# Optimization experiments

Hardware: AMD Instinct MI355X
Metric: run time of the kernel (lower is better)

## Reference

```python
import jax, jax.numpy as jnp
import numpy as np

N, E, H, ED = 50000, 400000, 512, 64
BN_EPS = 1e-5


def setup_inputs() -> dict:
    key = jax.random.key(0)
    ks = jax.random.split(key, 8)
    s = lambda d: 1.0 / np.sqrt(d)
    return {
        "x": jax.random.normal(ks[0], (N, H), jnp.float32),
        "edge_attr": jax.random.normal(ks[1], (E, ED), jnp.float32),
        "edge_index": jax.random.randint(ks[2], (2, E), 0, N, jnp.int32),
        # GINEConv edge projection (edge_dim -> hidden_dim)
        "W_e": jax.random.normal(ks[3], (ED, H), jnp.float32) * s(ED),
        "b_e": jnp.zeros((H,), jnp.float32),
        # 2-layer MLP: Linear(H, 2H) -> BN -> SiLU -> Linear(2H, H)
        "W1": jax.random.normal(ks[4], (H, 2 * H), jnp.float32) * s(H),
        "b1": jnp.zeros((2 * H,), jnp.float32),
        "g1": jnp.ones((2 * H,), jnp.float32),
        "beta1": jnp.zeros((2 * H,), jnp.float32),
        "W2": jax.random.normal(ks[5], (2 * H, H), jnp.float32) * s(2 * H),
        "b2": jnp.zeros((H,), jnp.float32),
        # outer BatchNorm(hidden_dim)
        "g2": jnp.ones((H,), jnp.float32),
        "beta2": jnp.zeros((H,), jnp.float32),
        # trainable GIN epsilon (init 0)
        "eps": jnp.zeros((), jnp.float32),
    }


def _bn(h, g, b):
    # training-mode batch norm over the node dimension (biased variance)
    mu = jnp.mean(h, axis=0)
    var = jnp.mean(jnp.square(h - mu), axis=0)
    return (h - mu) * jax.lax.rsqrt(var + BN_EPS) * g + b


def reference(x, edge_attr, edge_index, W_e, b_e, W1, b1, g1, beta1, W2, b2, g2, beta2, eps):
    src, dst = edge_index[0], edge_index[1]
    # message: ReLU(x_j + lin(e_ij)), gathered per edge  -> [E, H]
    msg = jax.nn.relu(x[src] + edge_attr @ W_e + b_e)
    # scatter-add aggregate into destination nodes -> [N, H]
    aggr = jax.ops.segment_sum(msg, dst, num_segments=x.shape[0])
    # GIN combine + 2-layer MLP with internal BatchNorm + SiLU (dropout=0)
    h = (1.0 + eps) * x + aggr
    h = jax.nn.silu(_bn(h @ W1 + b1, g1, beta1))
    h = h @ W2 + b2
    # outer BatchNorm + SiLU (dropout=0 -> identity)
    return jax.nn.silu(_bn(h, g2, beta2))
```

## Files before the change

kernel.cpp:

```cpp
#include <hip/hip_runtime.h>
#include <math.h>

#define NN 50000
#define NE 400000
#define HD 512
#define EDIM 64
#define H2 1024
#define LDT 72
#define CAP_SLOT 1200000
#define CAP_TILE 75000
#define CAP_HEAVY 8192
#define NBLK_SCAN 98

typedef short s16x8 __attribute__((ext_vector_type(8)));
typedef float f32x4 __attribute__((ext_vector_type(4)));

__device__ __forceinline__ unsigned short f2bf(float f) {
    union { float f; unsigned u; } v; v.f = f;
    unsigned r = v.u + 0x7fffu + ((v.u >> 16) & 1u);
    return (unsigned short)(r >> 16);
}
__device__ __forceinline__ float bf2f(unsigned short h) {
    union { unsigned u; float f; } v; v.u = ((unsigned)h) << 16;
    return v.f;
}
__device__ __forceinline__ float silu_f(float t) {
    return t / (1.f + __expf(-t));
}
__device__ __forceinline__ void gload_lds16(const unsigned short* g, unsigned short* l) {
    __builtin_amdgcn_global_load_lds(
        (const __attribute__((address_space(1))) unsigned int*)(g),
        (__attribute__((address_space(3))) unsigned int*)(l), 16, 0, 0);
}

constexpr size_t OFF_AGGRC = 0;
constexpr size_t OFF_XB   = 16777216;
constexpr size_t OFF_H1   = 0;
constexpr size_t OFF_H    = 102400000;
constexpr size_t OFF_WET  = 153600000;
constexpr size_t OFF_W1T  = OFF_WET + 65536;
constexpr size_t OFF_W2T  = OFF_W1T + 1048576;
constexpr size_t OFF_CNT  = OFF_W2T + 1048576;
constexpr size_t OFF_B1S  = OFF_CNT + 200000;
constexpr size_t OFF_B1Q  = OFF_B1S + 4096;
constexpr size_t OFF_B2S  = OFF_B1Q + 4096;
constexpr size_t OFF_B2Q  = OFF_B2S + 2048;
constexpr size_t ZERO_BYTES = 200000 + 4096 + 4096 + 2048 + 2048;
constexpr size_t OFF_TEX  = OFF_B2Q + 2048;
constexpr size_t OFF_BSUM = OFF_TEX + 200000;
constexpr size_t OFF_BOFF = OFF_BSUM + 512;
constexpr size_t OFF_T    = OFF_BOFF + 512;
constexpr size_t OFF_CUR  = OFF_T + 64;
constexpr size_t OFF_NOT  = OFF_CUR + 200000;
constexpr size_t OFF_SRCP = OFF_NOT + 300032;
constexpr size_t OFF_EIXP = OFF_SRCP + 4800000;
constexpr size_t OFF_SC1  = OFF_EIXP + 4800000;
constexpr size_t OFF_SB1  = OFF_SC1 + 4096;
constexpr size_t OFF_SC2  = OFF_SB1 + 4096;
constexpr size_t OFF_SB2  = OFF_SC2 + 2048;

__global__ __launch_bounds__(256) void k_convert(const float* __restrict__ We,
    const float* __restrict__ W1, const float* __restrict__ W2,
    unsigned short* __restrict__ wet, unsigned short* __restrict__ w1t,
    unsigned short* __restrict__ w2t) {
    int i = blockIdx.x * 256 + threadIdx.x;
    if (i < 32768) {
        int n = i >> 6, k = i & 63;
        wet[i] = f2bf(We[k * HD + n]);
    } else if (i < 32768 + 524288) {
        int j = i - 32768;
        int n = j >> 9, k = j & 511;
        w1t[j] = f2bf(W1[k * H2 + n]);
    } else if (i < 32768 + 2 * 524288) {
        int j = i - (32768 + 524288);
        int n = j >> 10, k = j & 1023;
        w2t[j] = f2bf(W2[k * HD + n]);
    }
}

__global__ __launch_bounds__(256) void k_xconv(const float* __restrict__ x,
    unsigned short* __restrict__ xb) {
    int t = blockIdx.x * 256 + threadIdx.x;
    if (t >= NN * 64) return;
    int n = t >> 6, rem = t & 63;
    int cb = rem >> 4, l = rem & 15;
    const float* src = x + (size_t)n * HD + cb * 128 + l;
    unsigned short o[8];
    #pragma unroll
    for (int j = 0; j < 8; ++j) o[j] = f2bf(src[j * 16]);
    *(uint4*)(xb + (size_t)n * HD + cb * 128 + l * 8) = *(const uint4*)o;
}

__global__ __launch_bounds__(256) void k_hist(const int* __restrict__ dst, int* __restrict__ counts) {
    int e = blockIdx.x * 256 + threadIdx.x;
    if (e < NE) atomicAdd(&counts[dst[e]], 1);
}

__global__ __launch_bounds__(512) void k_scan1(const int* __restrict__ counts,
    int* __restrict__ tile_excl, int* __restrict__ bsum) {
    __shared__ int wsums[8];
    int b = blockIdx.x, t = threadIdx.x;
    int i = b * 512 + t;
    int v = (i < NN) ? ((counts[i] + 15) >> 4) : 0;
    int lane = t & 63, wid = t >> 6;
    int x = v;
    #pragma unroll
    for (int o = 1; o < 64; o <<= 1) {
        int y = __shfl_up(x, o, 64);
        if (lane >= o) x += y;
    }
    if (lane == 63) wsums[wid] = x;
    __syncthreads();
    if (t == 0) {
        int run = 0;
        for (int w = 0; w < 8; ++w) { int tmp = wsums[w]; wsums[w] = run; run += tmp; }
    }
    __syncthreads();
    int excl = x - v + wsums[wid];
    if (i < NN) tile_excl[i] = excl;
    if (t == 511) bsum[b] = excl + v;
}

__global__ void k_scan2(const int* __restrict__ bsum, int* __restrict__ boff, int* __restrict__ Tout) {
    if (threadIdx.x == 0) {
        int run = 0;
        for (int b = 0; b < NBLK_SCAN; ++b) { boff[b] = run; run += bsum[b]; }
        Tout[0] = run;
        Tout[1] = 0;
    }
}

__global__ __launch_bounds__(512) void k_scan3(const int* __restrict__ counts,
    int* __restrict__ tile_excl, const int* __restrict__ boff,
    int* __restrict__ cursor, int* __restrict__ node_of_tile, int* __restrict__ Tout) {
    int b = blockIdx.x, t = threadIdx.x;
    int i = b * 512 + t;
    if (i >= NN) return;
    int tc = (counts[i] + 15) >> 4;
    int ts = tile_excl[i] + boff[b];
    cursor[i] = ts * 16;
    int hid = -1;
    if (tc > 1) {
        hid = atomicAdd(&Tout[1], 1);
        if (hid >= CAP_HEAVY) hid = CAP_HEAVY - 1;
    }
    tile_excl[i] = hid;
    unsigned tag = (tc > 1) ? (0x80000000u | (unsigned)hid) : (unsigned)i;
    for (int k = 0; k < tc; ++k) node_of_tile[ts + k] = (int)tag;
}

__global__ __launch_bounds__(256) void k_scatter(const int* __restrict__ src, const int* __restrict__ dst,
    int* __restrict__ cursor, int* __restrict__ srcp, int* __restrict__ eidxp) {
    int e = blockIdx.x * 256 + threadIdx.x;
    if (e < NE) {
        int d = dst[e];
        int p = atomicAdd(&cursor[d], 1);
        srcp[p] = src[e];
        eidxp[p] = e;
    }
}

__global__ __launch_bounds__(256, 4) void k_edge(
    const float* __restrict__ ea, const unsigned short* __restrict__ wet,
    const unsigned short* __restrict__ xb, const float* __restrict__ b_e,
    const float* __restrict__ eps,
    const int* __restrict__ srcp, const int* __restrict__ eidxp,
    const int* __restrict__ node_of_tile, const int* __restrict__ Tptr,
    float* __restrict__ aggrc, unsigned short* __restrict__ h) {
    int tile0 = blockIdx.x * 2;
    int T = Tptr[0];
    if (tile0 >= T) return;
    __shared__ unsigned short As[32 * LDT];
    __shared__ int Ss[32];
    __shared__ float Rs[4][128];
    int t = threadIdx.x;
    int slot0 = tile0 * 16;
    {
        int r = t >> 3, qq = t & 7;
        int s = srcp[slot0 + r];
        if (qq == 0) Ss[r] = s;
        unsigned short* lp = As + r * LDT + qq * 8;
        if (s >= 0) {
            int eix = eidxp[slot0 + r];
            const float* gp = ea + (size_t)eix * EDIM + qq * 8;
            float4 v0 = ((const float4*)gp)[0];
            float4 v1 = ((const float4*)gp)[1];
            lp[0] = f2bf(v0.x); lp[1] = f2bf(v0.y); lp[2] = f2bf(v0.z); lp[3] = f2bf(v0.w);
            lp[4] = f2bf(v1.x); lp[5] = f2bf(v1.y); lp[6] = f2bf(v1.z); lp[7] = f2bf(v1.w);
        } else {
            uint4 z = {0u, 0u, 0u, 0u};
            *(uint4*)lp = z;
        }
    }
    __syncthreads();
    int wave = t >> 6, lane = t & 63, l15 = lane & 15, quad = lane >> 4;
    int cblk = wave * 128;
    f32x4 acc[2][8];
    #pragma unroll
    for (int i = 0; i < 2; ++i)
        #pragma unroll
        for (int j = 0; j < 8; ++j) acc[i][j] = (f32x4){0.f, 0.f, 0.f, 0.f};
    #pragma unroll
    for (int k0 = 0; k0 < 64; k0 += 32) {
        s16x8 af[2], bfr[8];
        #pragma unroll
        for (int i = 0; i < 2; ++i)
            af[i] = *(const s16x8*)(As + (i * 16 + l15) * LDT + k0 + quad * 8);
        #pragma unroll
        for (int j = 0; j < 8; ++j)
            bfr[j] = *(const s16x8*)(wet + (size_t)(cblk + j * 16 + l15) * EDIM + k0 + quad * 8);
        #pragma unroll
        for (int i = 0; i < 2; ++i)
            #pragma unroll
            for (int j = 0; j < 8; ++j)
                acc[i][j] = __builtin_amdgcn_mfma_f32_16x16x32_bf16(af[i], bfr[j], acc[i][j], 0, 0, 0);
    }
    float ep = 1.0f + eps[0];
    float bev[8];
    #pragma unroll
    for (int j = 0; j < 8; ++j) bev[j] = b_e[cblk + j * 16 + l15];
    float* rp = Rs[wave];
    #pragma unroll
    for (int i = 0; i < 2; ++i) {
        int tile = tile0 + i;
        unsigned meta = (unsigned)node_of_tile[tile];
        int v = (int)(meta & 0x7fffffffu);
        int vc = v < NN ? v : 0;
        int srow = i * 16 + quad * 4;
        s16x8 xr[4]; float msk[4];
        #pragma unroll
        for (int r = 0; r < 4; ++r) {
            int s = Ss[srow + r];
            msk[r] = s >= 0 ? 1.f : 0.f;
            xr[r] = *(const s16x8*)(xb + (size_t)(s >= 0 ? s : 0) * HD + cblk + l15 * 8);
        }
        s16x8 xo = *(const s16x8*)(xb + (size_t)vc * HD + cblk + l15 * 8);
        float sum8[8];
        #pragma unroll
        for (int j = 0; j < 8; ++j) sum8[j] = 0.f;
        #pragma unroll
        for (int r = 0; r < 4; ++r) {
            #pragma unroll
            for (int j = 0; j < 8; ++j) {
                float vv = acc[i][j][r] + bf2f((unsigned short)xr[r][j]) + bev[j];
                vv = vv > 0.f ? vv : 0.f;
                sum8[j] = fmaf(msk[r], vv, sum8[j]);
            }
        }
        #pragma unroll
        for (int j = 0; j < 8; ++j) {
            sum8[j] += __shfl_xor(sum8[j], 16, 64);
            sum8[j] += __shfl_xor(sum8[j], 32, 64);
        }
        if (tile < T) {
            if (meta & 0x80000000u) {
                if (quad == 0) {
                    float* ap = aggrc + (size_t)v * HD + cblk;
                    #pragma unroll
                    for (int j = 0; j < 8; ++j) atomicAdd(ap + j * 16 + l15, sum8[j]);
                }
            } else {
                int j0 = quad * 2, j1 = j0 + 1;
                rp[j0 * 16 + l15] = fmaf(ep, bf2f((unsigned short)xo[j0]), sum8[j0]);
                rp[j1 * 16 + l15] = fmaf(ep, bf2f((unsigned short)xo[j1]), sum8[j1]);
                unsigned pk = (unsigned)f2bf(rp[lane * 2]) |
                              ((unsigned)f2bf(rp[lane * 2 + 1]) << 16);
                *(unsigned*)(h + (size_t)v * HD + cblk + lane * 2) = pk;
            }
        }
    }
}

__global__ __launch_bounds__(256) void k_combine_heavy(const float* __restrict__ aggrc,
    const float* __restrict__ x, const int* __restrict__ counts, const int* __restrict__ hidmap,
    const float* __restrict__ eps, unsigned short* __restrict__ h) {
    long i = ((long)blockIdx.x * 256 + threadIdx.x) * 4;
    if (i >= (long)NN * HD) return;
    int v = (int)(i >> 9);
    int c = counts[v];
    if (c >= 1 && c <= 16) return;
    float ep = 1.0f + eps[0];
    float4 a = {0.f, 0.f, 0.f, 0.f};
    if (c > 16) a = *(const float4*)(aggrc + (size_t)hidmap[v] * HD + (i & (HD - 1)));
    float4 xv = *(const float4*)(x + i);
    uint2 p;
    p.x = (unsigned)f2bf(ep * xv.x + a.x) | ((unsigned)f2bf(ep * xv.y + a.y) << 16);
    p.y = (unsigned)f2bf(ep * xv.z + a.z) | ((unsigned)f2bf(ep * xv.w + a.w) << 16);
    *(uint2*)(h + i) = p;
}

template <bool BF16OUT, bool SILU_A>
__global__ __launch_bounds__(256) void k_gemm_bn(
    const unsigned short* __restrict__ A, const unsigned short* __restrict__ Bt,
    const float* __restrict__ bias, void* __restrict__ Cv,
    float* __restrict__ bn_sum, float* __restrict__ bn_sumsq,
    const float* __restrict__ a_sc, const float* __restrict__ a_sb,
    int M, int K, int Nn) {
    __shared__ unsigned short As[SILU_A ? (128 * LDT) : (128 * 64)];
    __shared__ unsigned short Bs[128 * 64];
    __shared__ float csum[128], csumsq[128];
    constexpr int LDA = SILU_A ? LDT : 64;
    int mblk = blockIdx.x, nblk = blockIdx.y;
    int t = threadIdx.x;
    int row0 = mblk * 128, col0 = nblk * 128;
    int wid = t >> 6, lane = t & 63, l15 = lane & 15, quad = lane >> 4;
    int rb = (lane >> 3), cb8 = (lane & 7) * 8;
    int scb8 = cb8 ^ (rb * 8);
    int rswz = (l15 & 7) * 8;
    f32x4 acc[2][8];
    #pragma unroll
    for (int i = 0; i < 2; ++i)
        #pragma unroll
        for (int j = 0; j < 8; ++j) acc[i][j] = (f32x4){0.f, 0.f, 0.f, 0.f};

    for (int k0 = 0; k0 < K; k0 += 64) {
        __syncthreads();
        #pragma unroll
        for (int c = 0; c < 4; ++c) {
            int row = wid * 32 + c * 8 + rb;
            gload_lds16(Bt + (size_t)(col0 + row) * K + k0 + scb8,
                        Bs + row * 64 + cb8);
        }
        if constexpr (!SILU_A) {
            #pragma unroll
            for (int c = 0; c < 4; ++c) {
                int row = wid * 32 + c * 8 + rb;
                gload_lds16(A + (size_t)(row0 + row) * K + k0 + scb8,
                            As + row * 64 + cb8);
            }
        } else {
            int r = t >> 1, half = t & 1;
            int row = row0 + r;
            int kb = k0 + half * 32;
            unsigned short* lp = As + r * LDT + half * 32;
            if (row < M) {
                const unsigned short* gp = A + (size_t)row * K + kb;
                #pragma unroll
                for (int jj = 0; jj < 4; ++jj) {
                    uint4 u = *(const uint4*)(gp + jj * 8);
                    float4 sA = *(const float4*)(a_sc + kb + jj * 8);
                    float4 sB = *(const float4*)(a_sc + kb + jj * 8 + 4);
                    float4 bA = *(const float4*)(a_sb + kb + jj * 8);
                    float4 bB = *(const float4*)(a_sb + kb + jj * 8 + 4);
                    unsigned short o[8];
                    o[0] = f2bf(silu_f(bf2f((unsigned short)(u.x & 0xffffu)) * sA.x + bA.x));
                    o[1] = f2bf(silu_f(bf2f((unsigned short)(u.x >> 16)) * sA.y + bA.y));
                    o[2] = f2bf(silu_f(bf2f((unsigned short)(u.y & 0xffffu)) * sA.z + bA.z));
                    o[3] = f2bf(silu_f(bf2f((unsigned short)(u.y >> 16)) * sA.w + bA.w));
                    o[4] = f2bf(silu_f(bf2f((unsigned short)(u.z & 0xffffu)) * sB.x + bB.x));
                    o[5] = f2bf(silu_f(bf2f((unsigned short)(u.z >> 16)) * sB.y + bB.y));
                    o[6] = f2bf(silu_f(bf2f((unsigned short)(u.w & 0xffffu)) * sB.z + bB.z));
                    o[7] = f2bf(silu_f(bf2f((unsigned short)(u.w >> 16)) * sB.w + bB.w));
                    #pragma unroll
                    for (int m = 0; m < 8; ++m) lp[jj * 8 + m] = o[m];
                }
            } else {
                uint4 z = {0u, 0u, 0u, 0u};
                #pragma unroll
                for (int jj = 0; jj < 4; ++jj) *(uint4*)(lp + jj * 8) = z;
            }
        }
        __syncthreads();
        #pragma unroll
        for (int kk = 0; kk < 64; kk += 32) {
            s16x8 af[2], bfr[8];
            #pragma unroll
            for (int i = 0; i < 2; ++i) {
                if constexpr (SILU_A)
                    af[i] = *(const s16x8*)(As + (wid * 32 + i * 16 + l15) * LDA + kk + quad * 8);
                else
                    af[i] = *(const s16x8*)(As + (wid * 32 + i * 16 + l15) * 64 + ((kk + quad * 8) ^ rswz));
            }
            #pragma unroll
            for (int j = 0; j < 8; ++j)
                bfr[j] = *(const s16x8*)(Bs + (j * 16 + l15) * 64 + ((kk + quad * 8) ^ rswz));
            #pragma unroll
            for (int i = 0; i < 2; ++i)
                #pragma unroll
                for (int j = 0; j < 8; ++j)
                    acc[i][j] = __builtin_amdgcn_mfma_f32_16x16x32_bf16(af[i], bfr[j], acc[i][j], 0, 0, 0);
        }
    }
    if (t < 128) { csum[t] = 0.f; csumsq[t] = 0.f; }
    __syncthreads();
    int mrow0 = row0 + wid * 32;
    #pragma unroll
    for (int j = 0; j < 8; ++j) {
        int col = j * 16 + l15;
        float bv = bias[col0 + col];
        float ls = 0.f, lq = 0.f;
        #pragma unroll
        for (int i = 0; i < 2; ++i) {
            #pragma unroll
            for (int r = 0; r < 4; ++r) {
                int row = mrow0 + i * 16 + quad * 4 + r;
                if (row < M) {
                    float v = acc[i][j][r] + bv;
                    if (BF16OUT)
                        ((unsigned short*)Cv)[(size_t)row * Nn + col0 + col] = f2bf(v);
                    else
                        ((float*)Cv)[(size_t)row * Nn + col0 + col] = v;
                    ls += v; lq += v * v;
                }
            }
        }
        ls += __shfl_xor(ls, 16, 64); ls += __shfl_xor(ls, 32, 64);
        lq += __shfl_xor(lq, 16, 64); lq += __shfl_xor(lq, 32, 64);
        if (quad == 0) {
            atomicAdd(&csum[col], ls);
            atomicAdd(&csumsq[col], lq);
        }
    }
    __syncthreads();
    if (t < 128) {
        atomicAdd(bn_sum + col0 + t, csum[t]);
        atomicAdd(bn_sumsq + col0 + t, csumsq[t]);
    }
}

__global__ __launch_bounds__(256) void k_bn_final(const float* __restrict__ s,
    const float* __restrict__ q, const float* __restrict__ g, const float* __restrict__ beta,
    float* __restrict__ scale, float* __restrict__ sbias, int C, float invN) {
    int c = blockIdx.x * 256 + threadIdx.x;
    if (c < C) {
        float mu = s[c] * invN;
        float var = q[c] * invN - mu * mu;
        var = fmaxf(var, 0.f);
        float sc = g[c] * rsqrtf(var + 1e-5f);
        scale[c] = sc;
        sbias[c] = beta[c] - mu * sc;
    }
}

__global__ __launch_bounds__(256) void k_out(float* __restrict__ out,
    const float* __restrict__ sc, const float* __restrict__ sb, long total) {
    long i = ((long)blockIdx.x * 256 + threadIdx.x) * 4;
    if (i >= total) return;
    int c = (int)(i & (HD - 1));
    float4 v = *(const float4*)(out + i);
    float4 s4 = *(const float4*)(sc + c);
    float4 b4 = *(const float4*)(sb + c);
    float4 o;
    o.x = silu_f(v.x * s4.x + b4.x);
    o.y = silu_f(v.y * s4.y + b4.y);
    o.z = silu_f(v.z * s4.z + b4.z);
    o.w = silu_f(v.w * s4.w + b4.w);
    *(float4*)(out + i) = o;
}

extern "C" void kernel_launch(void* const* d_in, const int* in_sizes, int n_in,
                              void* d_out, int out_size, void* d_ws, size_t ws_size,
                              hipStream_t stream) {
    const float* x      = (const float*)d_in[0];
    const float* ea     = (const float*)d_in[1];
    const int*   ei     = (const int*)d_in[2];
    const float* W_e    = (const float*)d_in[3];
    const float* b_e    = (const float*)d_in[4];
    const float* W1     = (const float*)d_in[5];
    const float* b1     = (const float*)d_in[6];
    const float* g1     = (const float*)d_in[7];
    const float* beta1  = (const float*)d_in[8];
    const float* W2     = (const float*)d_in[9];
    const float* b2     = (const float*)d_in[10];
    const float* g2     = (const float*)d_in[11];
    const float* beta2  = (const float*)d_in[12];
    const float* eps    = (const float*)d_in[13];
    float* out = (float*)d_out;
    char* ws = (char*)d_ws;

    float*          aggrc = (float*)(ws + OFF_AGGRC);
    unsigned short* xb   = (unsigned short*)(ws + OFF_XB);
    unsigned short* h1   = (unsigned short*)(ws + OFF_H1);
    unsigned short* h    = (unsigned short*)(ws + OFF_H);
    unsigned short* wet  = (unsigned short*)(ws + OFF_WET);
    unsigned short* w1t  = (unsigned short*)(ws + OFF_W1T);
    unsigned short* w2t  = (unsigned short*)(ws + OFF_W2T);
    int* counts  = (int*)(ws + OFF_CNT);
    float* b1s   = (float*)(ws + OFF_B1S);
    float* b1q   = (float*)(ws + OFF_B1Q);
    float* b2s   = (float*)(ws + OFF_B2S);
    float* b2q   = (float*)(ws + OFF_B2Q);
    int* tex     = (int*)(ws + OFF_TEX);
    int* bsum    = (int*)(ws + OFF_BSUM);
    int* boff    = (int*)(ws + OFF_BOFF);
    int* Tptr    = (int*)(ws + OFF_T);
    int* cursor  = (int*)(ws + OFF_CUR);
    int* notile  = (int*)(ws + OFF_NOT);
    int* srcp    = (int*)(ws + OFF_SRCP);
    int* eidxp   = (int*)(ws + OFF_EIXP);
    float* sc1   = (float*)(ws + OFF_SC1);
    float* sb1   = (float*)(ws + OFF_SB1);
    float* sc2   = (float*)(ws + OFF_SC2);
    float* sb2   = (float*)(ws + OFF_SB2);

    hipMemsetAsync(aggrc, 0, (size_t)CAP_HEAVY * HD * 4, stream);
    hipMemsetAsync(ws + OFF_CNT, 0, ZERO_BYTES, stream);
    hipMemsetAsync(srcp, 0xFF, (size_t)CAP_SLOT * 4, stream);
    k_convert<<<4224, 256, 0, stream>>>(W_e, W1, W2, wet, w1t, w2t);
    k_xconv<<<(NN * 64 + 255) / 256, 256, 0, stream>>>(x, xb);
    k_hist<<<(NE + 255) / 256, 256, 0, stream>>>(ei + NE, counts);
    k_scan1<<<NBLK_SCAN, 512, 0, stream>>>(counts, tex, bsum);
    k_scan2<<<1, 64, 0, stream>>>(bsum, boff, Tptr);
    k_scan3<<<NBLK_SCAN, 512, 0, stream>>>(counts, tex, boff, cursor, notile, Tptr);
    k_scatter<<<(NE + 255) / 256, 256, 0, stream>>>(ei, ei + NE, cursor, srcp, eidxp);
    k_edge<<<CAP_TILE / 2, 256, 0, stream>>>(ea, wet, xb, b_e, eps, srcp, eidxp, notile, Tptr, aggrc, h);
    k_combine_heavy<<<(int)(((long)NN * HD / 4 + 255) / 256), 256, 0, stream>>>(
        aggrc, x, counts, tex, eps, h);
    k_gemm_bn<true, false><<<dim3((NN + 127) / 128, H2 / 128), 256, 0, stream>>>(
        h, w1t, b1, h1, b1s, b1q, nullptr, nullptr, NN, HD, H2);
    k_bn_final<<<4, 256, 0, stream>>>(b1s, b1q, g1, beta1, sc1, sb1, H2, 1.f / NN);
    k_gemm_bn<false, true><<<dim3((NN + 127) / 128, HD / 128), 256, 0, stream>>>(
        h1, w2t, b2, out, b2s, b2q, sc1, sb1, NN, H2, HD);
    k_bn_final<<<2, 256, 0, stream>>>(b2s, b2q, g2, beta2, sc2, sb2, HD, 1.f / NN);
    k_out<<<(int)(((long)NN * HD / 4 + 255) / 256), 256, 0, stream>>>(out, sc2, sb2, (long)NN * HD);
}
```

Baseline: 1.001 ms.

## Double-buffer LDS tiles in GEMM-BN kernels and swap grid order

Both MLP GEMMs now keep two LDS buffers for the A and B tiles, issuing the loads for the next K-step before the MFMA loop on the current one. This uses one barrier per step instead of two and hides global-load latency. The SiLU path holds the next A tile in registers and writes it after compute. The grid is also transposed so blocks sharing an A row-tile launch together, which should improve L2 reuse of A. The cost is doubled LDS and more registers, which may lower occupancy.

```diff
diff --git a/kernel.cpp b/kernel.cpp
--- a/kernel.cpp
+++ b/kernel.cpp
@@ -296,91 +296,124 @@
     float* __restrict__ bn_sum, float* __restrict__ bn_sumsq,
     const float* __restrict__ a_sc, const float* __restrict__ a_sb,
     int M, int K, int Nn) {
-    __shared__ unsigned short As[SILU_A ? (128 * LDT) : (128 * 64)];
-    __shared__ unsigned short Bs[128 * 64];
+    constexpr int LDA = SILU_A ? LDT : 64;
+    __shared__ unsigned short As[2][SILU_A ? (128 * LDT) : (128 * 64)];
+    __shared__ unsigned short Bs[2][128 * 64];
     __shared__ float csum[128], csumsq[128];
-    constexpr int LDA = SILU_A ? LDT : 64;
-    int mblk = blockIdx.x, nblk = blockIdx.y;
+    int nblk = blockIdx.x, mblk = blockIdx.y;
     int t = threadIdx.x;
     int row0 = mblk * 128, col0 = nblk * 128;
     int wid = t >> 6, lane = t & 63, l15 = lane & 15, quad = lane >> 4;
     int rb = (lane >> 3), cb8 = (lane & 7) * 8;
     int scb8 = cb8 ^ (rb * 8);
     int rswz = (l15 & 7) * 8;
+    int ar = t >> 1, ahalf = t & 1;
+    int arow = row0 + ar;
     f32x4 acc[2][8];
     #pragma unroll
     for (int i = 0; i < 2; ++i)
         #pragma unroll
         for (int j = 0; j < 8; ++j) acc[i][j] = (f32x4){0.f, 0.f, 0.f, 0.f};
 
-    for (int k0 = 0; k0 < K; k0 += 64) {
-        __syncthreads();
+    auto stageB = [&](int buf, int k0) {
         #pragma unroll
         for (int c = 0; c < 4; ++c) {
             int row = wid * 32 + c * 8 + rb;
             gload_lds16(Bt + (size_t)(col0 + row) * K + k0 + scb8,
-                        Bs + row * 64 + cb8);
-        }
-        if constexpr (!SILU_A) {
-            #pragma unroll
-            for (int c = 0; c < 4; ++c) {
-                int row = wid * 32 + c * 8 + rb;
-                gload_lds16(A + (size_t)(row0 + row) * K + k0 + scb8,
-                            As + row * 64 + cb8);
-            }
-        } else {
-            int r = t >> 1, half = t & 1;
-            int row = row0 + r;
-            int kb = k0 + half * 32;
-            unsigned short* lp = As + r * LDT + half * 32;
-            if (row < M) {
-                const unsigned short* gp = A + (size_t)row * K + kb;
-                #pragma unroll
-                for (int jj = 0; jj < 4; ++jj) {
-                    uint4 u = *(const uint4*)(gp + jj * 8);
-                    float4 sA = *(const float4*)(a_sc + kb + jj * 8);
-                    float4 sB = *(const float4*)(a_sc + kb + jj * 8 + 4);
-                    float4 bA = *(const float4*)(a_sb + kb + jj * 8);
-                    float4 bB = *(const float4*)(a_sb + kb + jj * 8 + 4);
-                    unsigned short o[8];
-                    o[0] = f2bf(silu_f(bf2f((unsigned short)(u.x & 0xffffu)) * sA.x + bA.x));
-                    o[1] = f2bf(silu_f(bf2f((unsigned short)(u.x >> 16)) * sA.y + bA.y));
-                    o[2] = f2bf(silu_f(bf2f((unsigned short)(u.y & 0xffffu)) * sA.z + bA.z));
-                    o[3] = f2bf(silu_f(bf2f((unsigned short)(u.y >> 16)) * sA.w + bA.w));
-                    o[4] = f2bf(silu_f(bf2f((unsigned short)(u.z & 0xffffu)) * sB.x + bB.x));
-                    o[5] = f2bf(silu_f(bf2f((unsigned short)(u.z >> 16)) * sB.y + bB.y));
-                    o[6] = f2bf(silu_f(bf2f((unsigned short)(u.w & 0xffffu)) * sB.z + bB.z));
-                    o[7] = f2bf(silu_f(bf2f((unsigned short)(u.w >> 16)) * sB.w + bB.w));
-                    #pragma unroll
-                    for (int m = 0; m < 8; ++m) lp[jj * 8 + m] = o[m];
-                }
+                        Bs[buf] + row * 64 + cb8);
+        }
+    };
+    auto stageA_g = [&](int buf, int k0) {
+        #pragma unroll
+        for (int c = 0; c < 4; ++c) {
+            int row = wid * 32 + c * 8 + rb;
+            gload_lds16(A + (size_t)(row0 + row) * K + k0 + scb8,
+                        As[buf] + row * 64 + cb8);
+        }
+    };
+    auto loadA_regs = [&](int k0, uint4* au) {
+        const unsigned short* gp = A + (size_t)arow * K + k0 + ahalf * 32;
+        #pragma unroll
+        for (int jj = 0; jj < 4; ++jj) {
+            uint4 z = {0u, 0u, 0u, 0u};
+            au[jj] = (arow < M) ? *(const uint4*)(gp + jj * 8) : z;
+        }
+    };
+    auto writeA_silu = [&](int buf, int k0, const uint4* au) {
+        int kb = k0 + ahalf * 32;
+        unsigned short* lp = As[buf] + ar * LDT + ahalf * 32;
+        #pragma unroll
+        for (int jj = 0; jj < 4; ++jj) {
+            uint4 u = au[jj];
+            float4 sA = *(const float4*)(a_sc + kb + jj * 8);
+            float4 sB = *(const float4*)(a_sc + kb + jj * 8 + 4);
+            float4 bA = *(const float4*)(a_sb + kb + jj * 8);
+            float4 bB = *(const float4*)(a_sb + kb + jj * 8 + 4);
+            unsigned short o[8];
+            o[0] = f2bf(silu_f(bf2f((unsigned short)(u.x & 0xffffu)) * sA.x + bA.x));
+            o[1] = f2bf(silu_f(bf2f((unsigned short)(u.x >> 16)) * sA.y + bA.y));
+            o[2] = f2bf(silu_f(bf2f((unsigned short)(u.y & 0xffffu)) * sA.z + bA.z));
+            o[3] = f2bf(silu_f(bf2f((unsigned short)(u.y >> 16)) * sA.w + bA.w));
+            o[4] = f2bf(silu_f(bf2f((unsigned short)(u.z & 0xffffu)) * sB.x + bB.x));
+            o[5] = f2bf(silu_f(bf2f((unsigned short)(u.z >> 16)) * sB.y + bB.y));
+            o[6] = f2bf(silu_f(bf2f((unsigned short)(u.w & 0xffffu)) * sB.z + bB.z));
+            o[7] = f2bf(silu_f(bf2f((unsigned short)(u.w >> 16)) * sB.w + bB.w));
+            if (arow < M) {
+                for (int m = 0; m < 8; ++m) lp[jj * 8 + m] = o[m];
             } else {
                 uint4 z = {0u, 0u, 0u, 0u};
-                #pragma unroll
-                for (int jj = 0; jj < 4; ++jj) *(uint4*)(lp + jj * 8) = z;
+                *(uint4*)(lp + jj * 8) = z;
             }
         }
-        __syncthreads();
+    };
+
+    stageB(0, 0);
+    if constexpr (!SILU_A) {
+        stageA_g(0, 0);
+    } else {
+        uint4 au0[4];
+        loadA_regs(0, au0);
+        writeA_silu(0, 0, au0);
+    }
+    __syncthreads();
+
+    int cur = 0;
+    int nsteps = K >> 6;
+    for (int s = 0; s < nsteps; ++s) {
+        bool hn = (s + 1) < nsteps;
+        int k0n = (s + 1) << 6;
+        uint4 au[4];
+        if (hn) {
+            stageB(cur ^ 1, k0n);
+            if constexpr (!SILU_A) stageA_g(cur ^ 1, k0n);
+            else loadA_regs(k0n, au);
+        }
         #pragma unroll
         for (int kk = 0; kk < 64; kk += 32) {
             s16x8 af[2], bfr[8];
             #pragma unroll
             for (int i = 0; i < 2; ++i) {
                 if constexpr (SILU_A)
-                    af[i] = *(const s16x8*)(As + (wid * 32 + i * 16 + l15) * LDA + kk + quad * 8);
+                    af[i] = *(const s16x8*)(As[cur] + (wid * 32 + i * 16 + l15) * LDA + kk + quad * 8);
                 else
-                    af[i] = *(const s16x8*)(As + (wid * 32 + i * 16 + l15) * 64 + ((kk + quad * 8) ^ rswz));
+                    af[i] = *(const s16x8*)(As[cur] + (wid * 32 + i * 16 + l15) * 64 + ((kk + quad * 8) ^ rswz));
             }
             #pragma unroll
             for (int j = 0; j < 8; ++j)
-                bfr[j] = *(const s16x8*)(Bs + (j * 16 + l15) * 64 + ((kk + quad * 8) ^ rswz));
+                bfr[j] = *(const s16x8*)(Bs[cur] + (j * 16 + l15) * 64 + ((kk + quad * 8) ^ rswz));
             #pragma unroll
             for (int i = 0; i < 2; ++i)
                 #pragma unroll
                 for (int j = 0; j < 8; ++j)
                     acc[i][j] = __builtin_amdgcn_mfma_f32_16x16x32_bf16(af[i], bfr[j], acc[i][j], 0, 0, 0);
         }
-    }
+        if (hn) {
+            if constexpr (SILU_A) writeA_silu(cur ^ 1, k0n, au);
+        }
+        __syncthreads();
+        cur ^= 1;
+    }
+
     if (t < 128) { csum[t] = 0.f; csumsq[t] = 0.f; }
     __syncthreads();
     int mrow0 = row0 + wid * 32;
@@ -506,10 +539,10 @@
     k_edge<<<CAP_TILE / 2, 256, 0, stream>>>(ea, wet, xb, b_e, eps, srcp, eidxp, notile, Tptr, aggrc, h);
     k_combine_heavy<<<(int)(((long)NN * HD / 4 + 255) / 256), 256, 0, stream>>>(
         aggrc, x, counts, tex, eps, h);
-    k_gemm_bn<true, false><<<dim3((NN + 127) / 128, H2 / 128), 256, 0, stream>>>(
+    k_gemm_bn<true, false><<<dim3(H2 / 128, (NN + 127) / 128), 256, 0, stream>>>(
         h, w1t, b1, h1, b1s, b1q, nullptr, nullptr, NN, HD, H2);
     k_bn_final<<<4, 256, 0, stream>>>(b1s, b1q, g1, beta1, sc1, sb1, H2, 1.f / NN);
-    k_gemm_bn<false, true><<<dim3((NN + 127) / 128, HD / 128), 256, 0, stream>>>(
+    k_gemm_bn<false, true><<<dim3(HD / 128, (NN + 127) / 128), 256, 0, stream>>>(
         h1, w2t, b2, out, b2s, b2q, sc1, sb1, NN, H2, HD);
     k_bn_final<<<2, 256, 0, stream>>>(b2s, b2q, g2, beta2, sc2, sb2, HD, 1.f / NN);
     k_out<<<(int)(((long)NN * HD / 4 + 255) / 256), 256, 0, stream>>>(out, sc2, sb2, (long)NN * HD);
```

Result: slower. 1.172 ms (+17.1%).
